# Kernel tuning notes

Hardware: AMD Instinct MI355X
Metric: run time of the kernel (lower is better)

The kernel has to match this reference:

```python
import jax, jax.numpy as jnp
import numpy as np

N_NODES = 50000
N_EDGES = 800000
IN_C = 116
HEADS = 4
OUT_C = 16
OUT_DIM = HEADS * OUT_C  # 64
NUM_GRAPHS = 100
NEG_SLOPE = 0.2
BN_EPS = 1e-5


def setup_inputs() -> dict:
    key = jax.random.key(0)
    ks = jax.random.split(key, 16)
    x = jax.random.normal(ks[0], (N_NODES, IN_C), dtype=jnp.float32)
    edge_index = jax.random.randint(ks[1], (2, N_EDGES), 0, N_NODES, dtype=jnp.int32)
    edge_attr = jax.random.normal(ks[2], (N_EDGES, 1), dtype=jnp.float32)
    batch = jnp.sort(jax.random.randint(ks[3], (N_NODES,), 0, NUM_GRAPHS, dtype=jnp.int32))
    s = 0.1
    return {
        "x": x, "edge_index": edge_index, "edge_attr": edge_attr, "batch": batch,
        "Wl": jax.random.normal(ks[4], (IN_C, OUT_DIM)) * s,
        "bl": jnp.zeros((OUT_DIM,), jnp.float32),
        "Wr": jax.random.normal(ks[5], (IN_C, OUT_DIM)) * s,
        "br": jnp.zeros((OUT_DIM,), jnp.float32),
        "We": jax.random.normal(ks[6], (1, OUT_DIM)) * s,
        "att": jax.random.normal(ks[7], (HEADS, OUT_C)) * s,
        "gat_bias": jnp.zeros((OUT_DIM,), jnp.float32),
        "gamma": jnp.ones((OUT_DIM,), jnp.float32),
        "beta": jnp.zeros((OUT_DIM,), jnp.float32),
        "Wres": jax.random.normal(ks[8], (IN_C, OUT_DIM)) * s,
        "bres": jnp.zeros((OUT_DIM,), jnp.float32),
        "W1": jax.random.normal(ks[9], (OUT_DIM, 64)) * s,
        "b1": jnp.zeros((64,), jnp.float32),
        "W2": jax.random.normal(ks[10], (64, 2)) * s,
        "b2": jnp.zeros((2,), jnp.float32),
    }


def _gatv2(x, edge_index, edge_attr, Wl, bl, Wr, br, We, att, gat_bias):
    N = x.shape[0]
    # linear transforms (PyG lin_l applies to source/message, lin_r to target)
    xl = (x @ Wl + bl).reshape(N, HEADS, OUT_C)
    xr = (x @ Wr + br).reshape(N, HEADS, OUT_C)
    # add self loops with fill_value=1.0 for edge_attr
    loops = jnp.arange(N, dtype=edge_index.dtype)
    src = jnp.concatenate([edge_index[0], loops])
    dst = jnp.concatenate([edge_index[1], loops])
    ea = jnp.concatenate([edge_attr, jnp.ones((N, 1), edge_attr.dtype)], axis=0)
    edge_emb = (ea @ We).reshape(-1, HEADS, OUT_C)          # [E+N, H, C]
    # GATv2 scores: att . leaky_relu(xl_j + xr_i + edge_emb)
    e = jax.nn.leaky_relu(xl[src] + xr[dst] + edge_emb, NEG_SLOPE)
    logits = jnp.einsum('ehc,hc->eh', e, att)                # [E+N, H]
    # segment softmax over incoming edges of each target node
    m = jax.ops.segment_max(logits, dst, num_segments=N)     # [N, H]
    ex = jnp.exp(logits - m[dst])
    denom = jax.ops.segment_sum(ex, dst, num_segments=N)     # [N, H]
    alpha = ex / denom[dst]
    # weighted scatter-add of source messages
    out = jax.ops.segment_sum(alpha[:, :, None] * xl[src], dst, num_segments=N)
    return out.reshape(N, OUT_DIM) + gat_bias


def reference(x, edge_index, edge_attr, batch, Wl, bl, Wr, br, We, att, gat_bias,
              gamma, beta, Wres, bres, W1, b1, W2, b2):
    h = _gatv2(x, edge_index, edge_attr, Wl, bl, Wr, br, We, att, gat_bias)
    # BatchNorm1d (training-style batch statistics over node dim)
    mu = jnp.mean(h, axis=0)
    var = jnp.var(h, axis=0)
    h = gamma * (h - mu) * jax.lax.rsqrt(var + BN_EPS) + beta
    # residual projection of original features
    h = h + (x @ Wres + bres)
    # global mean pool per graph
    sums = jax.ops.segment_sum(h, batch, num_segments=NUM_GRAPHS)
    cnts = jax.ops.segment_sum(jnp.ones((h.shape[0],), h.dtype), batch, num_segments=NUM_GRAPHS)
    pooled = sums / jnp.maximum(cnts, 1.0)[:, None]          # [G, 64]
    # 2-layer predictor with ReLU between
    z = jax.nn.relu(pooled @ W1 + b1)
    return z @ W2 + b2                                       # [G, 2]
```

## Files before the change

kernel.cpp:

```cpp
#include <hip/hip_runtime.h>
#include <hip/hip_bf16.h>

#define IN_C 116
#define HEADS 4
#define OUT_C 16
#define OUT_DIM 64
#define NEG_SLOPE 0.2f
#define BN_EPS 1e-5f
#define LIN_BM 64
#define LIN_PAD 68
#define CAP 64
#define OVF_CAP 4096

__global__ __launch_bounds__(256) void lin3_kernel(
    const float* __restrict__ x,
    const float* __restrict__ Wl, const float* __restrict__ bl,
    const float* __restrict__ Wr, const float* __restrict__ br,
    const float* __restrict__ Wres, const float* __restrict__ bres,
    float* __restrict__ xl, float* __restrict__ xr, float* __restrict__ xres,
    int N)
{
    __shared__ float xsT[IN_C * LIN_PAD];
    const int bn = blockIdx.x * LIN_BM;
    const int tid = threadIdx.x;

    for (int i = tid; i < LIN_BM * IN_C; i += 256) {
        int n = i / IN_C, k = i - n * IN_C;
        int gn = bn + n;
        xsT[k * LIN_PAD + n] = (gn < N) ? x[(size_t)gn * IN_C + k] : 0.f;
    }
    __syncthreads();

    const int j = tid & 63;
    const int t = tid >> 6;
    const int nbase = 16 * t;

    float al[16], ar[16], as_[16];
    #pragma unroll
    for (int u = 0; u < 16; ++u) { al[u] = 0.f; ar[u] = 0.f; as_[u] = 0.f; }

    #pragma unroll 2
    for (int k = 0; k < IN_C; ++k) {
        const float* row = &xsT[k * LIN_PAD + nbase];
        float4 xa = *(const float4*)(row);
        float4 xb = *(const float4*)(row + 4);
        float4 xc = *(const float4*)(row + 8);
        float4 xd = *(const float4*)(row + 12);
        float wl  = Wl[k * OUT_DIM + j];
        float wr  = Wr[k * OUT_DIM + j];
        float wsv = Wres[k * OUT_DIM + j];
        float xv[16] = {xa.x, xa.y, xa.z, xa.w, xb.x, xb.y, xb.z, xb.w,
                        xc.x, xc.y, xc.z, xc.w, xd.x, xd.y, xd.z, xd.w};
        #pragma unroll
        for (int u = 0; u < 16; ++u) {
            al[u]  += xv[u] * wl;
            ar[u]  += xv[u] * wr;
            as_[u] += xv[u] * wsv;
        }
    }

    float blj = bl[j], brj = br[j], bsj = bres[j];
    #pragma unroll
    for (int u = 0; u < 16; ++u) {
        int gn = bn + nbase + u;
        if (gn < N) {
            xl[(size_t)gn * OUT_DIM + j]   = al[u] + blj;
            xr[(size_t)gn * OUT_DIM + j]   = ar[u] + brj;
            xres[(size_t)gn * OUT_DIM + j] = as_[u] + bsj;
        }
    }
}

__global__ __launch_bounds__(256) void fill_kernel(
    const int* __restrict__ ei, const float* __restrict__ ea,
    int* __restrict__ cnt, unsigned long long* __restrict__ epack,
    int* __restrict__ ovf, int* __restrict__ ovf_cnt, int E)
{
    int e = blockIdx.x * 256 + threadIdx.x;
    if (e >= E) return;
    int src = ei[e];
    int dst = ei[E + e];
    float av = ea[e];
    int slot = atomicAdd(&cnt[dst], 1);
    if (slot < CAP) {
        unsigned long long v =
            ((unsigned long long)(unsigned)__float_as_uint(av) << 32) | (unsigned)src;
        __builtin_nontemporal_store(v, epack + (size_t)dst * CAP + slot);
    } else {
        int o = atomicAdd(ovf_cnt, 1);
        if (o < OVF_CAP) {
            ovf[3 * o] = src; ovf[3 * o + 1] = __float_as_int(av); ovf[3 * o + 2] = dst;
        }
    }
}

__global__ __launch_bounds__(256) void gat_gather_kernel(
    const int* __restrict__ cnt, const unsigned long long* __restrict__ epack,
    const int* __restrict__ ovf, const int* __restrict__ ovf_cnt,
    const float* __restrict__ xl, float* __restrict__ xr_hout,
    const float* __restrict__ We, const float* __restrict__ att,
    const float* __restrict__ gat_bias, int N)
{
    const int lane = threadIdx.x & 63;
    const int wv   = threadIdx.x >> 6;
    const int g    = lane >> 4;
    const int q    = lane & 15;
    const int n = blockIdx.x * 16 + wv * 4 + g;
    if (n >= N) return;

    const float4 xr4 = *(const float4*)(xr_hout + (size_t)n * OUT_DIM + 4 * q);
    const float4 We4 = *(const float4*)(We + 4 * q);
    const float4 at4 = *(const float4*)(att + 4 * q);

    int len = cnt[n];
    len = len < CAP ? len : CAP;
    const unsigned long long* ep = epack + (size_t)n * CAP;

    float den, acc0, acc1, acc2, acc3;
    {
        float4 xv = *(const float4*)(xl + (size_t)n * OUT_DIM + 4 * q);
        float s0 = xv.x + xr4.x + We4.x;
        float s1 = xv.y + xr4.y + We4.y;
        float s2 = xv.z + xr4.z + We4.z;
        float s3 = xv.w + xr4.w + We4.w;
        s0 = s0 > 0.f ? s0 : NEG_SLOPE * s0;
        s1 = s1 > 0.f ? s1 : NEG_SLOPE * s1;
        s2 = s2 > 0.f ? s2 : NEG_SLOPE * s2;
        s3 = s3 > 0.f ? s3 : NEG_SLOPE * s3;
        float pl = at4.x * s0 + at4.y * s1 + at4.z * s2 + at4.w * s3;
        pl += __shfl_xor(pl, 1);
        pl += __shfl_xor(pl, 2);
        float ex = __expf(pl);
        den = ex;
        acc0 = ex * xv.x; acc1 = ex * xv.y; acc2 = ex * xv.z; acc3 = ex * xv.w;
    }

#define EDGE_CORE(SRC, AV)                                              \
    {                                                                   \
        int src = (SRC);                                                \
        float av = (AV);                                                \
        float4 xv = *(const float4*)(xl + (size_t)src * OUT_DIM + 4*q); \
        float s0 = xv.x + xr4.x + av * We4.x;                           \
        float s1 = xv.y + xr4.y + av * We4.y;                           \
        float s2 = xv.z + xr4.z + av * We4.z;                           \
        float s3 = xv.w + xr4.w + av * We4.w;                           \
        s0 = s0 > 0.f ? s0 : NEG_SLOPE * s0;                            \
        s1 = s1 > 0.f ? s1 : NEG_SLOPE * s1;                            \
        s2 = s2 > 0.f ? s2 : NEG_SLOPE * s2;                            \
        s3 = s3 > 0.f ? s3 : NEG_SLOPE * s3;                            \
        float pl = at4.x * s0 + at4.y * s1 + at4.z * s2 + at4.w * s3;   \
        pl += __shfl_xor(pl, 1);                                        \
        pl += __shfl_xor(pl, 2);                                        \
        float ex = __expf(pl);                                          \
        den += ex;                                                      \
        acc0 += ex * xv.x;                                              \
        acc1 += ex * xv.y;                                              \
        acc2 += ex * xv.z;                                              \
        acc3 += ex * xv.w;                                              \
    }

#define EDGE_BODY(PP)                                                   \
    {                                                                   \
        unsigned long long v = __builtin_nontemporal_load(ep + (PP));   \
        EDGE_CORE((int)(unsigned)(v & 0xffffffffull),                   \
                  __uint_as_float((unsigned)(v >> 32)));                \
    }

    int p = 0;
    while (p + 4 <= len) {
        EDGE_BODY(p);
        EDGE_BODY(p + 1);
        EDGE_BODY(p + 2);
        EDGE_BODY(p + 3);
        p += 4;
    }
    while (p < len) { EDGE_BODY(p); ++p; }

    int oc = *ovf_cnt;
    if (oc > 0) {
        oc = oc < OVF_CAP ? oc : OVF_CAP;
        for (int o = 0; o < oc; ++o) {
            if (ovf[3 * o + 2] == n)
                EDGE_CORE(ovf[3 * o], __int_as_float(ovf[3 * o + 1]));
        }
    }
#undef EDGE_BODY
#undef EDGE_CORE

    const float4 bias4 = *(const float4*)(gat_bias + 4 * q);
    float inv = 1.0f / den;
    float4 o;
    o.x = acc0 * inv + bias4.x;
    o.y = acc1 * inv + bias4.y;
    o.z = acc2 * inv + bias4.z;
    o.w = acc3 * inv + bias4.w;
    *(float4*)(xr_hout + (size_t)n * OUT_DIM + 4 * q) = o;
}

__global__ __launch_bounds__(256) void stats_kernel(
    const float* __restrict__ h, float* __restrict__ chansum,
    float* __restrict__ chansumsq, int N)
{
    const int j = threadIdx.x & 63;
    const int t = threadIdx.x >> 6;
    float s = 0.f, ss = 0.f;
    for (int n = blockIdx.x * 4 + t; n < N; n += gridDim.x * 4) {
        float v = h[(size_t)n * OUT_DIM + j];
        s += v; ss += v * v;
    }
    __shared__ float ls[4][64], lss[4][64];
    ls[t][j] = s; lss[t][j] = ss;
    __syncthreads();
    if (t == 0) {
        atomicAdd(&chansum[j],   ls[0][j] + ls[1][j] + ls[2][j] + ls[3][j]);
        atomicAdd(&chansumsq[j], lss[0][j] + lss[1][j] + lss[2][j] + lss[3][j]);
    }
}

__global__ __launch_bounds__(256) void bn_res_pool_kernel(
    const float* __restrict__ hraw, const float* __restrict__ xres,
    const float* __restrict__ chansum, const float* __restrict__ chansumsq,
    const float* __restrict__ gamma, const float* __restrict__ beta,
    const int* __restrict__ batch,
    float* __restrict__ pooled, float* __restrict__ cnt, int N)
{
    const int j = threadIdx.x & 63;
    const int t = threadIdx.x >> 6;
    const int base = blockIdx.x * 256;
    const float invN = 1.0f / (float)N;
    const float mj = chansum[j] * invN;
    const float var = chansumsq[j] * invN - mj * mj;
    const float rj = rsqrtf(var + BN_EPS);
    const float gj = gamma[j], bj = beta[j];

    float sum = 0.f, c = 0.f;
    int gcur = -1;
    for (int i = t; i < 256; i += 4) {
        int n = base + i;
        if (n >= N) break;
        int g = batch[n];
        if (g != gcur) {
            if (gcur >= 0) {
                atomicAdd(&pooled[gcur * OUT_DIM + j], sum);
                if (j == 0) atomicAdd(&cnt[gcur], c);
            }
            sum = 0.f; c = 0.f; gcur = g;
        }
        float v = gj * (hraw[(size_t)n * OUT_DIM + j] - mj) * rj + bj
                + xres[(size_t)n * OUT_DIM + j];
        sum += v; c += 1.f;
    }
    if (gcur >= 0) {
        atomicAdd(&pooled[gcur * OUT_DIM + j], sum);
        if (j == 0) atomicAdd(&cnt[gcur], c);
    }
}

__global__ __launch_bounds__(64) void mlp_kernel(
    const float* __restrict__ pooled, const float* __restrict__ cnt,
    const float* __restrict__ W1, const float* __restrict__ b1,
    const float* __restrict__ W2, const float* __restrict__ b2,
    float* __restrict__ out, int G)
{
    int g = blockIdx.x, j = threadIdx.x;
    __shared__ float ps[64];
    float c = cnt[g];
    c = c > 1.0f ? c : 1.0f;
    ps[j] = pooled[g * OUT_DIM + j] / c;
    __syncthreads();
    float z = b1[j];
    for (int k = 0; k < 64; ++k) z += ps[k] * W1[k * 64 + j];
    z = z > 0.f ? z : 0.f;
    float o0 = z * W2[j * 2 + 0];
    float o1 = z * W2[j * 2 + 1];
    #pragma unroll
    for (int off = 32; off > 0; off >>= 1) {
        o0 += __shfl_down(o0, off);
        o1 += __shfl_down(o1, off);
    }
    if (j == 0) {
        out[g * 2 + 0] = o0 + b2[0];
        out[g * 2 + 1] = o1 + b2[1];
    }
}

extern "C" void kernel_launch(void* const* d_in, const int* in_sizes, int n_in,
                              void* d_out, int out_size, void* d_ws, size_t ws_size,
                              hipStream_t stream) {
    const float* x        = (const float*)d_in[0];
    const int*   ei       = (const int*)d_in[1];
    const float* ea       = (const float*)d_in[2];
    const int*   batch    = (const int*)d_in[3];
    const float* Wl       = (const float*)d_in[4];
    const float* bl       = (const float*)d_in[5];
    const float* Wr       = (const float*)d_in[6];
    const float* br       = (const float*)d_in[7];
    const float* We       = (const float*)d_in[8];
    const float* att      = (const float*)d_in[9];
    const float* gat_bias = (const float*)d_in[10];
    const float* gamma    = (const float*)d_in[11];
    const float* beta     = (const float*)d_in[12];
    const float* Wres     = (const float*)d_in[13];
    const float* bres     = (const float*)d_in[14];
    const float* W1       = (const float*)d_in[15];
    const float* b1       = (const float*)d_in[16];
    const float* W2       = (const float*)d_in[17];
    const float* b2       = (const float*)d_in[18];
    float* out = (float*)d_out;

    const int N = in_sizes[0] / IN_C;
    const int E = in_sizes[1] / 2;
    const int G = out_size / 2;

    float* ws = (float*)d_ws;
    float* xl      = ws;
    float* xr      = xl + (size_t)N * OUT_DIM;
    float* xres    = xr + (size_t)N * OUT_DIM;
    unsigned long long* epack =
        (unsigned long long*)(xres + (size_t)N * OUT_DIM);
    int*   cnt     = (int*)(epack + (size_t)N * CAP);
    int*   ovf_cnt = cnt + N;
    float* chansum   = (float*)(ovf_cnt + 1);
    float* chansumsq = chansum + 64;
    float* pooled    = chansumsq + 64;
    float* cntg      = pooled + (size_t)G * OUT_DIM;
    int*   ovf       = (int*)(cntg + G);

    size_t zero_bytes = (size_t)((char*)(cntg + G) - (char*)cnt);
    hipMemsetAsync(cnt, 0, zero_bytes, stream);

    lin3_kernel<<<(N + LIN_BM - 1) / LIN_BM, 256, 0, stream>>>(
        x, Wl, bl, Wr, br, Wres, bres, xl, xr, xres, N);

    fill_kernel<<<(E + 255) / 256, 256, 0, stream>>>(
        ei, ea, cnt, epack, ovf, ovf_cnt, E);

    gat_gather_kernel<<<(N + 15) / 16, 256, 0, stream>>>(
        cnt, epack, ovf, ovf_cnt, xl, xr, We, att, gat_bias, N);

    stats_kernel<<<256, 256, 0, stream>>>(xr, chansum, chansumsq, N);

    bn_res_pool_kernel<<<(N + 255) / 256, 256, 0, stream>>>(
        xr, xres, chansum, chansumsq, gamma, beta, batch, pooled, cntg, N);

    mlp_kernel<<<G, 64, 0, stream>>>(pooled, cntg, W1, b1, W2, b2, out, G);
}
```

Measured before the change: 307.0 us.

## Fuse linear projections and edge bucketing into one XCD-aware prep kernel

Merges the three-matrix linear kernel and the edge fill kernel into one launch whose blocks are interleaved (every fifth block does linear work at a smaller node tile). Fill blocks are assigned by block index mod 8 to a node partition, so destination atomics and epack writes for each partition stay in one XCD's L2. The price is every fill block re-reading its edge range's dst indices and skipping edges outside its partition (8x redundant reads of dst). The gather loop is also unrolled by 8 instead of 4, and epack stores become normal instead of nontemporal.

```diff
diff --git a/kernel.cpp b/kernel.cpp
--- a/kernel.cpp
+++ b/kernel.cpp
@@ -7,89 +7,104 @@
 #define OUT_DIM 64
 #define NEG_SLOPE 0.2f
 #define BN_EPS 1e-5f
-#define LIN_BM 64
-#define LIN_PAD 68
+#define LIN_BM 32
+#define LIN_PAD 36
 #define CAP 64
 #define OVF_CAP 4096
-
-__global__ __launch_bounds__(256) void lin3_kernel(
+#define CYCLE 40
+
+__global__ __launch_bounds__(256) void prep_kernel(
     const float* __restrict__ x,
     const float* __restrict__ Wl, const float* __restrict__ bl,
     const float* __restrict__ Wr, const float* __restrict__ br,
     const float* __restrict__ Wres, const float* __restrict__ bres,
     float* __restrict__ xl, float* __restrict__ xr, float* __restrict__ xres,
-    int N)
-{
-    __shared__ float xsT[IN_C * LIN_PAD];
-    const int bn = blockIdx.x * LIN_BM;
-    const int tid = threadIdx.x;
-
-    for (int i = tid; i < LIN_BM * IN_C; i += 256) {
-        int n = i / IN_C, k = i - n * IN_C;
-        int gn = bn + n;
-        xsT[k * LIN_PAD + n] = (gn < N) ? x[(size_t)gn * IN_C + k] : 0.f;
-    }
-    __syncthreads();
-
-    const int j = tid & 63;
-    const int t = tid >> 6;
-    const int nbase = 16 * t;
-
-    float al[16], ar[16], as_[16];
-    #pragma unroll
-    for (int u = 0; u < 16; ++u) { al[u] = 0.f; ar[u] = 0.f; as_[u] = 0.f; }
-
-    #pragma unroll 2
-    for (int k = 0; k < IN_C; ++k) {
-        const float* row = &xsT[k * LIN_PAD + nbase];
-        float4 xa = *(const float4*)(row);
-        float4 xb = *(const float4*)(row + 4);
-        float4 xc = *(const float4*)(row + 8);
-        float4 xd = *(const float4*)(row + 12);
-        float wl  = Wl[k * OUT_DIM + j];
-        float wr  = Wr[k * OUT_DIM + j];
-        float wsv = Wres[k * OUT_DIM + j];
-        float xv[16] = {xa.x, xa.y, xa.z, xa.w, xb.x, xb.y, xb.z, xb.w,
-                        xc.x, xc.y, xc.z, xc.w, xd.x, xd.y, xd.z, xd.w};
-        #pragma unroll
-        for (int u = 0; u < 16; ++u) {
-            al[u]  += xv[u] * wl;
-            ar[u]  += xv[u] * wr;
-            as_[u] += xv[u] * wsv;
-        }
-    }
-
-    float blj = bl[j], brj = br[j], bsj = bres[j];
-    #pragma unroll
-    for (int u = 0; u < 16; ++u) {
-        int gn = bn + nbase + u;
-        if (gn < N) {
-            xl[(size_t)gn * OUT_DIM + j]   = al[u] + blj;
-            xr[(size_t)gn * OUT_DIM + j]   = ar[u] + brj;
-            xres[(size_t)gn * OUT_DIM + j] = as_[u] + bsj;
-        }
-    }
-}
-
-__global__ __launch_bounds__(256) void fill_kernel(
     const int* __restrict__ ei, const float* __restrict__ ea,
     int* __restrict__ cnt, unsigned long long* __restrict__ epack,
-    int* __restrict__ ovf, int* __restrict__ ovf_cnt, int E)
-{
-    int e = blockIdx.x * 256 + threadIdx.x;
-    if (e >= E) return;
-    int src = ei[e];
-    int dst = ei[E + e];
-    float av = ea[e];
-    int slot = atomicAdd(&cnt[dst], 1);
-    if (slot < CAP) {
-        unsigned long long v =
-            ((unsigned long long)(unsigned)__float_as_uint(av) << 32) | (unsigned)src;
-        __builtin_nontemporal_store(v, epack + (size_t)dst * CAP + slot);
+    int* __restrict__ ovf, int* __restrict__ ovf_cnt,
+    int N, int E, int NBLIN, int FPP, int PART)
+{
+    __shared__ float xsT[IN_C * LIN_PAD];
+    const int b = blockIdx.x;
+    const int tid = threadIdx.x;
+
+    if (b % 5 == 4) {
+        const int lb = (b / CYCLE) * 8 + (b % CYCLE) / 5;
+        if (lb >= NBLIN) return;
+        const int bn = lb * LIN_BM;
+
+        for (int i = tid; i < LIN_BM * IN_C; i += 256) {
+            int n = i / IN_C, k = i - n * IN_C;
+            int gn = bn + n;
+            xsT[k * LIN_PAD + n] = (gn < N) ? x[(size_t)gn * IN_C + k] : 0.f;
+        }
+        __syncthreads();
+
+        const int j = tid & 63;
+        const int t = tid >> 6;
+        const int nbase = 8 * t;
+
+        float al[8] = {0,0,0,0,0,0,0,0};
+        float ar[8] = {0,0,0,0,0,0,0,0};
+        float as_[8] = {0,0,0,0,0,0,0,0};
+
+        #pragma unroll 4
+        for (int k = 0; k < IN_C; ++k) {
+            float4 xa = *(const float4*)&xsT[k * LIN_PAD + nbase];
+            float4 xb = *(const float4*)&xsT[k * LIN_PAD + nbase + 4];
+            float wl  = Wl[k * OUT_DIM + j];
+            float wr  = Wr[k * OUT_DIM + j];
+            float wsv = Wres[k * OUT_DIM + j];
+            float xv[8] = {xa.x, xa.y, xa.z, xa.w, xb.x, xb.y, xb.z, xb.w};
+            #pragma unroll
+            for (int u = 0; u < 8; ++u) {
+                al[u]  += xv[u] * wl;
+                ar[u]  += xv[u] * wr;
+                as_[u] += xv[u] * wsv;
+            }
+        }
+
+        float blj = bl[j], brj = br[j], bsj = bres[j];
+        #pragma unroll
+        for (int u = 0; u < 8; ++u) {
+            int gn = bn + nbase + u;
+            if (gn < N) {
+                xl[(size_t)gn * OUT_DIM + j]   = al[u] + blj;
+                xr[(size_t)gn * OUT_DIM + j]   = ar[u] + brj;
+                xres[(size_t)gn * OUT_DIM + j] = as_[u] + bsj;
+            }
+        }
     } else {
-        int o = atomicAdd(ovf_cnt, 1);
-        if (o < OVF_CAP) {
-            ovf[3 * o] = src; ovf[3 * o + 1] = __float_as_int(av); ovf[3 * o + 2] = dst;
+        const int c = b & 7;
+        const int cyc  = b / CYCLE;
+        const int jcur = ((b % CYCLE) - c) >> 3;
+        const int jx   = (2 * ((4 - c + 5) % 5)) % 5;
+        const int q    = jcur - (jx < jcur ? 1 : 0);
+        const int r    = cyc * 4 + q;
+
+        const int lo = c * PART;
+        const int hi = (lo + PART < N) ? lo + PART : N;
+        const unsigned span = (unsigned)(hi - lo);
+
+        long long e0 = (long long)r * E / FPP;
+        long long e1 = (long long)(r + 1) * E / FPP;
+
+        for (long long e = e0 + tid; e < e1; e += 256) {
+            int dst = ei[E + e];
+            if ((unsigned)(dst - lo) >= span) continue;
+            int src = ei[e];
+            float av = ea[e];
+            int slot = atomicAdd(&cnt[dst], 1);
+            if (slot < CAP) {
+                unsigned long long v =
+                    ((unsigned long long)(unsigned)__float_as_uint(av) << 32) | (unsigned)src;
+                epack[(size_t)dst * CAP + slot] = v;
+            } else {
+                int o = atomicAdd(ovf_cnt, 1);
+                if (o < OVF_CAP) {
+                    ovf[3 * o] = src; ovf[3 * o + 1] = __float_as_int(av); ovf[3 * o + 2] = dst;
+                }
+            }
         }
     }
 }
@@ -167,14 +182,15 @@
     }
 
     int p = 0;
-    while (p + 4 <= len) {
-        EDGE_BODY(p);
-        EDGE_BODY(p + 1);
-        EDGE_BODY(p + 2);
-        EDGE_BODY(p + 3);
-        p += 4;
-    }
-    while (p < len) { EDGE_BODY(p); ++p; }
+    while (p + 8 <= len) {
+        EDGE_BODY(p);     EDGE_BODY(p + 1);
+        EDGE_BODY(p + 2); EDGE_BODY(p + 3);
+        EDGE_BODY(p + 4); EDGE_BODY(p + 5);
+        EDGE_BODY(p + 6); EDGE_BODY(p + 7);
+        p += 8;
+    }
+    while (p + 2 <= len) { EDGE_BODY(p); EDGE_BODY(p + 1); p += 2; }
+    if (p < len) EDGE_BODY(p);
 
     int oc = *ovf_cnt;
     if (oc > 0) {
@@ -329,11 +345,15 @@
     size_t zero_bytes = (size_t)((char*)(cntg + G) - (char*)cnt);
     hipMemsetAsync(cnt, 0, zero_bytes, stream);
 
-    lin3_kernel<<<(N + LIN_BM - 1) / LIN_BM, 256, 0, stream>>>(
-        x, Wl, bl, Wr, br, Wres, bres, xl, xr, xres, N);
-
-    fill_kernel<<<(E + 255) / 256, 256, 0, stream>>>(
-        ei, ea, cnt, epack, ovf, ovf_cnt, E);
+    const int NBLIN = (N + LIN_BM - 1) / LIN_BM;
+    const int CYC   = (NBLIN + 7) / 8;
+    const int T     = CYC * CYCLE;
+    const int FPP   = CYC * 4;
+    const int PART  = (N + 7) / 8;
+
+    prep_kernel<<<T, 256, 0, stream>>>(
+        x, Wl, bl, Wr, br, Wres, bres, xl, xr, xres,
+        ei, ea, cnt, epack, ovf, ovf_cnt, N, E, NBLIN, FPP, PART);
 
     gat_gather_kernel<<<(N + 15) / 16, 256, 0, stream>>>(
         cnt, epack, ovf, ovf_cnt, xl, xr, We, att, gat_bias, N);
```

After: 271.0 us. 11.7% less time.
